# Performance work log

Measured on AMD Instinct MI355X. Metric: run time of the kernel, lower is better.

Reference implementation:

```python
import jax, jax.numpy as jnp
import numpy as np

H = 1024          # hidden_size
NH = 16           # num_attention_heads
HD = H // NH      # head_dim = 64
CAUSAL_HEADS = 4  # causal_attention_heads
META_HEADS = NH // 4
B, S = 2, 2048
CVEC = 16
# static cognitive-state scalars (Python floats in the original dict)
CAUSAL_WEIGHT = 0.7   # > 0.5 -> causal branch active
AWARENESS = 0.9       # > 0.8 -> metacognitive branch active


def _mha(x, in_w, in_b, out_w, out_b, n_heads):
    """torch nn.MultiheadAttention (batch_first, self-attn, no mask, eval).
    in_w: [H, 3H] (pre-transposed), out_w: [H, H]."""
    b, s, h = x.shape
    hd = h // n_heads
    qkv = x @ in_w + in_b                      # [b, s, 3H]
    q, k, v = jnp.split(qkv, 3, axis=-1)
    def heads(t):
        return t.reshape(b, s, n_heads, hd).transpose(0, 2, 1, 3)  # [b, nh, s, hd]
    q, k, v = heads(q), heads(k), heads(v)
    scores = jnp.einsum('bhqd,bhkd->bhqk', q, k) / jnp.sqrt(jnp.float32(hd))
    probs = jax.nn.softmax(scores, axis=-1)
    ctx = jnp.einsum('bhqk,bhkd->bhqd', probs, v)
    ctx = ctx.transpose(0, 2, 1, 3).reshape(b, s, h)
    return ctx @ out_w + out_b


def setup_inputs() -> dict:
    key = jax.random.key(0)
    ks = jax.random.split(key, 20)
    w = lambda k, shp: (jax.random.normal(k, shp, dtype=jnp.float32) * 0.02)
    inp = {
        'hidden_states': jax.random.normal(ks[0], (B, S, H), dtype=jnp.float32),
        'attention_mask': jnp.ones((B, S), dtype=jnp.int32),
        'consciousness_vector': jax.random.uniform(ks[1], (CVEC,), dtype=jnp.float32),
        'Wq': w(ks[2], (H, H)), 'bq': jnp.zeros((H,), jnp.float32),
        'Wk': w(ks[3], (H, H)), 'bk': jnp.zeros((H,), jnp.float32),
        'Wv': w(ks[4], (H, H)), 'bv': jnp.zeros((H,), jnp.float32),
        'Wg': w(ks[5], (H, NH)), 'bg': jnp.zeros((NH,), jnp.float32),
        'Wa': w(ks[6], (CVEC, NH)), 'ba': jnp.zeros((NH,), jnp.float32),
        'ca_in_w': w(ks[7], (H, 3 * H)), 'ca_in_b': jnp.zeros((3 * H,), jnp.float32),
        'ca_out_w': w(ks[8], (H, H)), 'ca_out_b': jnp.zeros((H,), jnp.float32),
        'ma_in_w': w(ks[9], (H, 3 * H)), 'ma_in_b': jnp.zeros((3 * H,), jnp.float32),
        'ma_out_w': w(ks[10], (H, H)), 'ma_out_b': jnp.zeros((H,), jnp.float32),
        'Wo': w(ks[11], (H, H)), 'bo': jnp.zeros((H,), jnp.float32),
    }
    return inp


def reference(hidden_states, attention_mask, consciousness_vector,
              Wq, bq, Wk, bk, Wv, bv, Wg, bg, Wa, ba,
              ca_in_w, ca_in_b, ca_out_w, ca_out_b,
              ma_in_w, ma_in_b, ma_out_w, ma_out_b, Wo, bo):
    b, s, h = hidden_states.shape
    def heads(t):
        return t.reshape(b, s, NH, HD).transpose(0, 2, 1, 3)  # [b, NH, s, HD]
    q = heads(hidden_states @ Wq + bq)
    k = heads(hidden_states @ Wk + bk)
    v = heads(hidden_states @ Wv + bv)
    scores = jnp.einsum('bhqd,bhkd->bhqk', q, k) / jnp.sqrt(jnp.float32(HD))
    # consciousness modulation: sigmoid(gate(hs) + awareness(cvec)) -> [b, s, NH]
    gate = hidden_states @ Wg + bg
    awareness = consciousness_vector @ Wa + ba            # [NH]
    modulation = jax.nn.sigmoid(gate + awareness)         # [b, s, NH]
    # per-head, per-query-row scaling of scores ([b, NH, s, 1])
    scores = scores * modulation.transpose(0, 2, 1)[:, :, :, None]
    # mask: [b, s] -> [b, 1, 1, s]; masked positions -> -inf before softmax
    scores = jnp.where(attention_mask[:, None, None, :] == 0, -jnp.inf, scores)
    probs = jax.nn.softmax(scores, axis=-1)
    # dropout is identity in eval mode
    ctx = jnp.einsum('bhqk,bhkd->bhqd', probs, v)
    ctx = ctx.transpose(0, 2, 1, 3).reshape(b, s, h)
    # causal branch (causal_active > 0.5)
    causal_ctx = _mha(hidden_states, ca_in_w, ca_in_b, ca_out_w, ca_out_b, CAUSAL_HEADS)
    ctx = ctx * (1.0 - CAUSAL_WEIGHT) + causal_ctx * CAUSAL_WEIGHT
    # metacognitive branch (awareness_level > 0.8)
    meta_ctx = _mha(ctx, ma_in_w, ma_in_b, ma_out_w, ma_out_b, META_HEADS)
    mw = (AWARENESS - 0.8) / 0.2
    ctx = ctx * (1.0 - mw * 0.3) + meta_ctx * (mw * 0.3)
    return ctx @ Wo + bo
```

## Files before the change

### kernel.cpp

```cpp
#include <hip/hip_runtime.h>
#include <math.h>

#define HDIM 1024
#define NHEAD 16
#define SEQ   2048
#define BATCH 2
#define NROWS (BATCH * SEQ)
#define NEG_INF (-__builtin_inff())

typedef unsigned short u16;
typedef float  f32x4  __attribute__((ext_vector_type(4)));
typedef short  short8 __attribute__((ext_vector_type(8)));
typedef _Float16 half8 __attribute__((ext_vector_type(8)));
typedef __fp16 fp16x2 __attribute__((ext_vector_type(2)));

__device__ __forceinline__ u16 f2bf(float x) {
    unsigned u = __float_as_uint(x);
    unsigned r = u + 0x7fffu + ((u >> 16) & 1u);
    return (u16)(r >> 16);
}
__device__ __forceinline__ float bf2f(u16 h) { return __uint_as_float(((unsigned)h) << 16); }
__device__ __forceinline__ u16 f2h(float x) { _Float16 h = (_Float16)x; return *(u16*)&h; }
__device__ __forceinline__ unsigned pkh(float a, float b) {
    fp16x2 h = __builtin_amdgcn_cvt_pkrtz(a, b);
    return __builtin_bit_cast(unsigned int, h);
}
__device__ __forceinline__ float ex2(float x) { return __builtin_amdgcn_exp2f(x); }

__global__ __launch_bounds__(256) void conv_f16(const float* __restrict__ src,
                                                u16* __restrict__ dst)
{
    int i8 = (blockIdx.x * 256 + threadIdx.x) * 8;
    float4 a = *(const float4*)&src[i8];
    float4 b = *(const float4*)&src[i8 + 4];
    u16 h[8] = {f2h(a.x), f2h(a.y), f2h(a.z), f2h(a.w),
                f2h(b.x), f2h(b.y), f2h(b.z), f2h(b.w)};
    uint4 p;
    p.x = h[0] | (h[1] << 16); p.y = h[2] | (h[3] << 16);
    p.z = h[4] | (h[5] << 16); p.w = h[6] | (h[7] << 16);
    *(uint4*)&dst[i8] = p;
}

__global__ __launch_bounds__(256) void mask_bias(const int* __restrict__ m,
                                                 float* __restrict__ mb)
{
    int i = blockIdx.x * 256 + threadIdx.x;
    mb[i] = m[i] ? -6.f : NEG_INF;
}

__global__ __launch_bounds__(256) void convW(const float* __restrict__ Wsrc, int ldw, int n0,
                                             int dst, u16* __restrict__ WTH, u16* __restrict__ WTL)
{
    __shared__ float tile[64][65];
    int t = threadIdx.x;
    int nb = blockIdx.x * 64, kb = blockIdx.y * 64;
    #pragma unroll
    for (int i = 0; i < 4; i++) {
        int r = (t >> 4) + i * 16, cg = t & 15;
        float4 v = *(const float4*)&Wsrc[(size_t)(kb + r) * ldw + n0 + nb + cg * 4];
        tile[r][cg * 4 + 0] = v.x; tile[r][cg * 4 + 1] = v.y;
        tile[r][cg * 4 + 2] = v.z; tile[r][cg * 4 + 3] = v.w;
    }
    __syncthreads();
    int n = t & 63, g0 = (t >> 6) * 2;
    #pragma unroll
    for (int gg = 0; gg < 2; gg++) {
        int g = g0 + gg;
        u16 hi[8], lo[8];
        #pragma unroll
        for (int u = 0; u < 8; u++) {
            float x = tile[g * 8 + u][n];
            hi[u] = f2bf(x); lo[u] = f2bf(x - bf2f(hi[u]));
        }
        size_t ob = (size_t)(dst + nb + n) * 1024 + kb + g * 8;
        uint4 ph, pl;
        ph.x = hi[0] | (hi[1] << 16); ph.y = hi[2] | (hi[3] << 16);
        ph.z = hi[4] | (hi[5] << 16); ph.w = hi[6] | (hi[7] << 16);
        pl.x = lo[0] | (lo[1] << 16); pl.y = lo[2] | (lo[3] << 16);
        pl.z = lo[4] | (lo[5] << 16); pl.w = lo[6] | (lo[7] << 16);
        *(uint4*)&WTH[ob] = ph;
        *(uint4*)&WTL[ob] = pl;
    }
}

__global__ __launch_bounds__(256) void convW3_f16(
    const float* __restrict__ w0, const float* __restrict__ w1, const float* __restrict__ w2,
    int ldw, int n0s, u16* __restrict__ WT)
{
    __shared__ float tile[64][65];
    int t = threadIdx.x;
    int z = blockIdx.z;
    const float* Wsrc = (z == 0) ? w0 : (z == 1) ? w1 : w2;
    int n0 = z * n0s, dst = z * 1024;
    int nb = blockIdx.x * 64, kb = blockIdx.y * 64;
    #pragma unroll
    for (int i = 0; i < 4; i++) {
        int r = (t >> 4) + i * 16, cg = t & 15;
        float4 v = *(const float4*)&Wsrc[(size_t)(kb + r) * ldw + n0 + nb + cg * 4];
        tile[r][cg * 4 + 0] = v.x; tile[r][cg * 4 + 1] = v.y;
        tile[r][cg * 4 + 2] = v.z; tile[r][cg * 4 + 3] = v.w;
    }
    __syncthreads();
    int n = t & 63, g0 = (t >> 6) * 2;
    #pragma unroll
    for (int gg = 0; gg < 2; gg++) {
        int g = g0 + gg;
        u16 h[8];
        #pragma unroll
        for (int u = 0; u < 8; u++) h[u] = f2h(tile[g * 8 + u][n]);
        size_t ob = (size_t)(dst + nb + n) * 1024 + kb + g * 8;
        uint4 p;
        p.x = h[0] | (h[1] << 16); p.y = h[2] | (h[3] << 16);
        p.z = h[4] | (h[5] << 16); p.w = h[6] | (h[7] << 16);
        *(uint4*)&WT[ob] = p;
    }
}

__global__ __launch_bounds__(256) void transpose_f16(
    const u16* __restrict__ in, u16* __restrict__ out)
{
    __shared__ u16 th[64][72];
    int t = threadIdx.x;
    int cb = blockIdx.x * 64;
    int rb = blockIdx.y * 64;
    {
        int r = t >> 2;
        #pragma unroll
        for (int i = 0; i < 2; i++) {
            int ck = (t & 3) + 4 * i;
            *(short8*)&th[r][ck * 8] = *(const short8*)&in[(size_t)(rb + r) * 3072 + 2048 + cb + ck * 8];
        }
    }
    __syncthreads();
    int c = t & 63, g0 = (t >> 6) * 2;
    #pragma unroll
    for (int gg = 0; gg < 2; gg++) {
        int g = g0 + gg;
        u16 hv[8];
        #pragma unroll
        for (int u = 0; u < 8; u++) hv[u] = th[g * 8 + u][c];
        size_t ob = (size_t)(cb + c) * NROWS + rb + g * 8;
        uint4 ph;
        ph.x = hv[0] | (hv[1] << 16); ph.y = hv[2] | (hv[3] << 16);
        ph.z = hv[4] | (hv[5] << 16); ph.w = hv[6] | (hv[7] << 16);
        *(uint4*)&out[ob] = ph;
    }
}

__global__ __launch_bounds__(256) void gate_f32(
    const float* __restrict__ hs, const float* __restrict__ Wg,
    const float* __restrict__ bg, const float* __restrict__ cvec,
    const float* __restrict__ Wa, const float* __restrict__ ba,
    float* __restrict__ mod)
{
    __shared__ float aw[16];
    int t = threadIdx.x;
    if (t < 16) {
        float s = ba[t];
        for (int i = 0; i < 16; i++) s = fmaf(cvec[i], Wa[i * 16 + t], s);
        aw[t] = s;
    }
    __syncthreads();
    int h = t & 15;
    int r = blockIdx.x * 16 + (t >> 4);
    const float* hrow = hs + (size_t)r * HDIM;
    float s = bg[h];
    for (int k = 0; k < HDIM; k++) s = fmaf(hrow[k], Wg[k * 16 + h], s);
    s += aw[h];
    mod[(size_t)r * 16 + h] = 1.f / (1.f + __expf(-s));
}

__global__ __launch_bounds__(256, 3) void gemm_f16(
    const u16* __restrict__ A, const u16* __restrict__ BT,
    const float* __restrict__ b0, const float* __restrict__ b1, const float* __restrict__ b2,
    u16* __restrict__ out, int M, int N, int K)
{
    __shared__ u16 aS[128][40], bS[128][40];
    int t = threadIdx.x;
    int l = t & 63, w = t >> 6;
    int lane15 = l & 15, quad = l >> 4;
    int wm = (w >> 1) * 64, wn = (w & 1) * 64;
    int m0 = blockIdx.y * 128, n0 = blockIdx.x * 128;
    int sr = t >> 1;
    f32x4 acc[4][4] = {};
    short8 pa[2], pb[2];
    auto pre = [&](int k0) {
        #pragma unroll
        for (int i = 0; i < 2; i++) {
            int ck = (t & 1) * 2 + i;
            pa[i] = *(const short8*)&A[(size_t)(m0 + sr) * K + k0 + ck * 8];
            pb[i] = *(const short8*)&BT[(size_t)(n0 + sr) * K + k0 + ck * 8];
        }
    };
    pre(0);
    for (int k0 = 0; k0 < K; k0 += 32) {
        __syncthreads();
        #pragma unroll
        for (int i = 0; i < 2; i++) {
            int ck = (t & 1) * 2 + i;
            *(short8*)&aS[sr][ck * 8] = pa[i];
            *(short8*)&bS[sr][ck * 8] = pb[i];
        }
        __syncthreads();
        if (k0 + 32 < K) pre(k0 + 32);
        half8 af[4], bf[4];
        #pragma unroll
        for (int mt = 0; mt < 4; mt++)
            af[mt] = *(const half8*)&aS[wm + mt * 16 + lane15][quad * 8];
        #pragma unroll
        for (int nt = 0; nt < 4; nt++)
            bf[nt] = *(const half8*)&bS[wn + nt * 16 + lane15][quad * 8];
        #pragma unroll
        for (int mt = 0; mt < 4; mt++)
            #pragma unroll
            for (int nt = 0; nt < 4; nt++)
                acc[mt][nt] = __builtin_amdgcn_mfma_f32_16x16x32_f16(af[mt], bf[nt], acc[mt][nt], 0, 0, 0);
    }
    #pragma unroll
    for (int nt = 0; nt < 4; nt++) {
        int col = n0 + wn + nt * 16 + lane15;
        const float* bsel = (col < 1024) ? b0 : (col < 2048) ? b1 : b2;
        float bv = bsel[col & 1023];
        #pragma unroll
        for (int mt = 0; mt < 4; mt++)
            #pragma unroll
            for (int reg = 0; reg < 4; reg++) {
                int row = m0 + wm + mt * 16 + quad * 4 + reg;
                out[(size_t)row * N + col] = f2h(acc[mt][nt][reg] + bv);
            }
    }
}

__global__ __launch_bounds__(256, 2) void gemm_bf3(
    const u16* __restrict__ AH, const u16* __restrict__ AL,
    const u16* __restrict__ BTH, const u16* __restrict__ BTL,
    const float* __restrict__ bias,
    const u16* __restrict__ CinH, const u16* __restrict__ CinL,
    float* __restrict__ outF, u16* __restrict__ outH, u16* __restrict__ outL,
    u16* __restrict__ outX,
    int M, int N, int K, float alpha, float beta, int omode)
{
    __shared__ u16 aH[128][40], aL[128][40], bH[128][40], bL[128][40];
    int t = threadIdx.x;
    int l = t & 63, w = t >> 6;
    int lane15 = l & 15, quad = l >> 4;
    int wm = (w >> 1) * 64, wn = (w & 1) * 64;
    int m0 = blockIdx.y * 128, n0 = blockIdx.x * 128;
    int sr = t >> 1;
    f32x4 acc[4][4] = {};
    short8 pah[2], pal[2], pbh[2], pbl[2];

    auto pre = [&](int k0) {
        #pragma unroll
        for (int i = 0; i < 2; i++) {
            int ck = (t & 1) * 2 + i;
            size_t ga = (size_t)(m0 + sr) * K + k0 + ck * 8;
            size_t gb = (size_t)(n0 + sr) * K + k0 + ck * 8;
            pah[i] = *(const short8*)&AH[ga];
            pal[i] = *(const short8*)&AL[ga];
            pbh[i] = *(const short8*)&BTH[gb];
            pbl[i] = *(const short8*)&BTL[gb];
        }
    };
    pre(0);
    for (int k0 = 0; k0 < K; k0 += 32) {
        __syncthreads();
        #pragma unroll
        for (int i = 0; i < 2; i++) {
            int ck = (t & 1) * 2 + i;
            *(short8*)&aH[sr][ck * 8] = pah[i];
            *(short8*)&aL[sr][ck * 8] = pal[i];
            *(short8*)&bH[sr][ck * 8] = pbh[i];
            *(short8*)&bL[sr][ck * 8] = pbl[i];
        }
        __syncthreads();
        if (k0 + 32 < K) pre(k0 + 32);
        short8 afh[4], afl[4], bfh[4], bfl[4];
        #pragma unroll
        for (int mt = 0; mt < 4; mt++) {
            int r = wm + mt * 16 + lane15;
            afh[mt] = *(const short8*)&aH[r][quad * 8];
            afl[mt] = *(const short8*)&aL[r][quad * 8];
        }
        #pragma unroll
        for (int nt = 0; nt < 4; nt++) {
            int r = wn + nt * 16 + lane15;
            bfh[nt] = *(const short8*)&bH[r][quad * 8];
            bfl[nt] = *(const short8*)&bL[r][quad * 8];
        }
        #pragma unroll
        for (int mt = 0; mt < 4; mt++)
            #pragma unroll
            for (int nt = 0; nt < 4; nt++) {
                acc[mt][nt] = __builtin_amdgcn_mfma_f32_16x16x32_bf16(afh[mt], bfh[nt], acc[mt][nt], 0, 0, 0);
                acc[mt][nt] = __builtin_amdgcn_mfma_f32_16x16x32_bf16(afh[mt], bfl[nt], acc[mt][nt], 0, 0, 0);
                acc[mt][nt] = __builtin_amdgcn_mfma_f32_16x16x32_bf16(afl[mt], bfh[nt], acc[mt][nt], 0, 0, 0);
            }
    }
    #pragma unroll
    for (int nt = 0; nt < 4; nt++) {
        int col = n0 + wn + nt * 16 + lane15;
        float bv = bias[col];
        #pragma unroll
        for (int mt = 0; mt < 4; mt++) {
            #pragma unroll
            for (int reg = 0; reg < 4; reg++) {
                int row = m0 + wm + mt * 16 + quad * 4 + reg;
                size_t idx = (size_t)row * N + col;
                float v = alpha * (acc[mt][nt][reg] + bv);
                if (beta != 0.f) v += beta * (bf2f(CinH[idx]) + bf2f(CinL[idx]));
                if (omode == 0) outF[idx] = v;
                else {
                    u16 hb = f2bf(v);
                    outH[idx] = hb;
                    outL[idx] = f2bf(v - bf2f(hb));
                }
                if (outX) outX[idx] = f2h(v);
            }
        }
    }
}

__global__ __launch_bounds__(256, 4) void attn_main(
    const u16* __restrict__ QKV, const u16* __restrict__ VT,
    const float* __restrict__ modp, const float* __restrict__ mbias, float scale,
    u16* __restrict__ outH, u16* __restrict__ outL)
{
    constexpr int NT = SEQ / 64;
    constexpr int LD = 3 * HDIM;
    __shared__ __align__(16) u16 kb[2][64][64];
    __shared__ __align__(16) u16 vb[2][64][64];
    __shared__ __align__(16) u16 st[4][16][64];

    int t = threadIdx.x, l = t & 63, w = t >> 6;
    int lane15 = l & 15, quad = l >> 4;
    int qt0 = blockIdx.x * 64, h = blockIdx.y, b = blockIdx.z;
    int bS_ = b * SEQ;
    int sr = t >> 2, ck0 = (t & 3) * 2;
    int swz = (lane15 & 7) << 3;

    half8 qf[2];
    {
        size_t qoff = (size_t)(bS_ + qt0 + w * 16 + lane15) * LD + h * 64 + quad * 8;
        qf[0] = *(const half8*)&QKV[qoff];
        qf[1] = *(const half8*)&QKV[qoff + 32];
    }
    float smod2 = scale * 1.44269504f *
                  modp[(size_t)(bS_ + qt0 + w * 16 + lane15) * NHEAD + h];
    float lst = 0.f;
    f32x4 o[4] = {};

    short8 phK[2], phV[2];
    auto loadKV = [&](int kt) {
        size_t baseK = (size_t)(bS_ + kt + sr) * LD + HDIM + h * 64;
        phK[0] = *(const short8*)&QKV[baseK + ck0 * 8];
        phK[1] = *(const short8*)&QKV[baseK + (ck0 + 1) * 8];
        size_t baseV = (size_t)(h * 64 + sr) * NROWS + bS_ + kt;
        phV[0] = *(const short8*)&VT[baseV + ck0 * 8];
        phV[1] = *(const short8*)&VT[baseV + (ck0 + 1) * 8];
    };
    auto stage = [&](int pb_) {
        #pragma unroll
        for (int i = 0; i < 2; i++) {
            int cw = (ck0 + i) ^ (sr & 7);
            *(short8*)&kb[pb_][sr][cw * 8] = phK[i];
            *(short8*)&vb[pb_][sr][cw * 8] = phV[i];
        }
    };

    loadKV(0);

    for (int it = 0; it < NT; it++) {
        int kt = it * 64, pb = it & 1;
        stage(pb);
        __syncthreads();
        if (it + 1 < NT) loadKV(kt + 64);
        f32x4 sacc[4] = {};
        #pragma unroll
        for (int ks = 0; ks < 2; ks++)
            #pragma unroll
            for (int nb = 0; nb < 4; nb++) {
                int r = nb * 16 + lane15;
                int cw = (ks * 4 + quad) ^ (r & 7);
                half8 kf = *(const half8*)&kb[pb][r][cw * 8];
                sacc[nb] = __builtin_amdgcn_mfma_f32_16x16x32_f16(kf, qf[ks], sacc[nb], 0, 0, 0);
            }
        #pragma unroll
        for (int nb = 0; nb < 4; nb++) {
            float4 mb = *(const float4*)&mbias[bS_ + kt + nb * 16 + quad * 4];
            float p0 = ex2(fmaf(sacc[nb][0], smod2, mb.x));
            float p1 = ex2(fmaf(sacc[nb][1], smod2, mb.y));
            float p2 = ex2(fmaf(sacc[nb][2], smod2, mb.z));
            float p3 = ex2(fmaf(sacc[nb][3], smod2, mb.w));
            lst += (p0 + p1) + (p2 + p3);
            uint2 u2;
            u2.x = pkh(p0, p1);
            u2.y = pkh(p2, p3);
            *(uint2*)&st[w][lane15][(nb * 16 + quad * 4) ^ swz] = u2;
        }
        half8 pf[2];
        #pragma unroll
        for (int ks = 0; ks < 2; ks++)
            pf[ks] = *(const half8*)&st[w][lane15][(ks * 32 + quad * 8) ^ swz];
        #pragma unroll
        for (int ks = 0; ks < 2; ks++)
            #pragma unroll
            for (int nb = 0; nb < 4; nb++) {
                int r = nb * 16 + lane15;
                int cw = (ks * 4 + quad) ^ (r & 7);
                half8 vv = *(const half8*)&vb[pb][r][cw * 8];
                o[nb] = __builtin_amdgcn_mfma_f32_16x16x32_f16(pf[ks], vv, o[nb], 0, 0, 0);
            }
    }
    lst += __shfl_xor(lst, 16, 64);
    lst += __shfl_xor(lst, 32, 64);
    #pragma unroll
    for (int reg = 0; reg < 4; reg++) {
        float lv = __shfl(lst, quad * 4 + reg, 64);
        float inv = (lv > 0.f) ? 1.f / lv : 0.f;
        int row = qt0 + w * 16 + quad * 4 + reg;
        size_t rbase = (size_t)(bS_ + row) * HDIM + h * 64;
        #pragma unroll
        for (int nb = 0; nb < 4; nb++) {
            float v = o[nb][reg] * inv;
            size_t idx = rbase + nb * 16 + lane15;
            u16 hb = f2bf(v);
            outH[idx] = hb;
            outL[idx] = f2bf(v - bf2f(hb));
        }
    }
}

template <int NC>
__global__ __launch_bounds__(256, 2) void attn_f16(
    const u16* __restrict__ QKV, const u16* __restrict__ VT,
    float scale, u16* __restrict__ outH, u16* __restrict__ outL, int ldo)
{
    constexpr int HDT = NC * 64;
    constexpr int NT  = (SEQ / 2) / 64;
    constexpr int LD  = 3 * HDIM;
    __shared__ __align__(16) u16 kbuf[2][2][64][64];
    __shared__ __align__(16) u16 st[4][16][68];
    __shared__ float xl[2][16];

    int t = threadIdx.x, l = t & 63, w = t >> 6;
    int lane15 = l & 15, quad = l >> 4;
    int g = w & 1, s = w >> 1;
    int t128 = t & 127, srow = t128 >> 1, ckb = (t128 & 1) * 4;
    int qt0 = blockIdx.x * 32, h = blockIdx.y, b = blockIdx.z;
    int bS = b * SEQ, kbeg = s * (SEQ / 2);

    half8 qf[NC][2];
    {
        size_t qoff = (size_t)(bS + qt0 + g * 16 + lane15) * LD + h * HDT + quad * 8;
        #pragma unroll
        for (int c = 0; c < NC; c++)
            #pragma unroll
            for (int ks = 0; ks < 2; ks++)
                qf[c][ks] = *(const half8*)&QKV[qoff + c * 64 + ks * 32];
    }
    float sc2 = scale * 1.44269504f;
    float lst = 0.f;
    f32x4 o[NC][4] = {};

    short8 phv[4];
    auto loadK = [&](int c, int kt) {
        size_t base = (size_t)(bS + kt + srow) * LD + HDIM + h * HDT + c * 64;
        #pragma unroll
        for (int i = 0; i < 4; i++) phv[i] = *(const short8*)&QKV[base + (ckb + i) * 8];
    };
    auto loadV = [&](int c, int kt) {
        size_t base = (size_t)(h * HDT + c * 64 + srow) * NROWS + bS + kt;
        #pragma unroll
        for (int i = 0; i < 4; i++) phv[i] = *(const short8*)&VT[base + (ckb + i) * 8];
    };
    auto stor = [&](int pb_) {
        #pragma unroll
        for (int i = 0; i < 4; i++) {
            int ck = ckb + i, cw = ck ^ (srow & 7);
            *(short8*)&kbuf[pb_][s][srow][cw * 8] = phv[i];
        }
    };

    loadK(0, kbeg);
    stor(0);
    loadK(1, kbeg);
    int pb = 0;

    for (int it = 0; it < NT; it++) {
        int kt = kbeg + it * 64;
        f32x4 sacc[4] = {};
        #pragma unroll
        for (int c = 0; c < NC; c++) {
            __syncthreads();
            stor(pb ^ 1);
            if (c + 2 < NC) loadK(c + 2, kt);
            else if (c + 2 < 2 * NC) loadV(c + 2 - NC, kt);
            else if (it + 1 < NT) loadK(0, kt + 64);
            #pragma unroll
            for (int ks = 0; ks < 2; ks++)
                #pragma unroll
                for (int nb = 0; nb < 4; nb++) {
                    int r = nb * 16 + lane15;
                    int cw = (ks * 4 + quad) ^ (r & 7);
                    half8 kf = *(const half8*)&kbuf[pb][s][r][cw * 8];
                    sacc[nb] = __builtin_amdgcn_mfma_f32_16x16x32_f16(kf, qf[c][ks], sacc[nb], 0, 0, 0);
                }
            pb ^= 1;
        }
        #pragma unroll
        for (int nb = 0; nb < 4; nb++) {
            float p0 = ex2(fmaf(sacc[nb][0], sc2, -6.f));
            float p1 = ex2(fmaf(sacc[nb][1], sc2, -6.f));
            float p2 = ex2(fmaf(sacc[nb][2], sc2, -6.f));
            float p3 = ex2(fmaf(sacc[nb][3], sc2, -6.f));
            lst += (p0 + p1) + (p2 + p3);
            uint2 u2;
            u2.x = pkh(p0, p1);
            u2.y = pkh(p2, p3);
            *(uint2*)&st[w][lane15][nb * 16 + quad * 4] = u2;
        }
        half8 pf[2];
        #pragma unroll
        for (int ks = 0; ks < 2; ks++)
            pf[ks] = *(const half8*)&st[w][lane15][ks * 32 + quad * 8];
        #pragma unroll
        for (int c = 0; c < NC; c++) {
            __syncthreads();
            if (it < NT - 1 || c < NC - 1) stor(pb ^ 1);
            if (c + 2 < NC) loadV(c + 2, kt);
            else if (it + 1 < NT) {
                int p2 = c + 2 - NC;
                if (p2 < NC) loadK(p2, kt + 64); else loadV(p2 - NC, kt + 64);
            }
            #pragma unroll
            for (int ks = 0; ks < 2; ks++)
                #pragma unroll
                for (int nb = 0; nb < 4; nb++) {
                    int r = nb * 16 + lane15;
                    int cw = (ks * 4 + quad) ^ (r & 7);
                    half8 vv = *(const half8*)&kbuf[pb][s][r][cw * 8];
                    o[c][nb] = __builtin_amdgcn_mfma_f32_16x16x32_f16(pf[ks], vv, o[c][nb], 0, 0, 0);
                }
            pb ^= 1;
        }
    }
    lst += __shfl_xor(lst, 16, 64);
    lst += __shfl_xor(lst, 32, 64);
    float* xO = (float*)kbuf;
    __syncthreads();
    if (s == 1) {
        #pragma unroll
        for (int c = 0; c < NC; c++)
            #pragma unroll
            for (int nb = 0; nb < 4; nb++)
                #pragma unroll
                for (int reg = 0; reg < 4; reg++)
                    xO[(size_t)(g * 16 + quad * 4 + reg) * HDT + c * 64 + nb * 16 + lane15] = o[c][nb][reg];
        if (quad == 0) xl[g][lane15] = lst;
    }
    __syncthreads();
    if (s == 0) {
        #pragma unroll
        for (int reg = 0; reg < 4; reg++) {
            float lt = __shfl(lst, quad * 4 + reg, 64) + xl[g][quad * 4 + reg];
            float inv = (lt > 0.f) ? 1.f / lt : 0.f;
            int row = qt0 + g * 16 + quad * 4 + reg;
            size_t rbase = (size_t)(bS + row) * ldo + h * HDT;
            #pragma unroll
            for (int c = 0; c < NC; c++)
                #pragma unroll
                for (int nb = 0; nb < 4; nb++) {
                    float x1 = xO[(size_t)(g * 16 + quad * 4 + reg) * HDT + c * 64 + nb * 16 + lane15];
                    float v = (o[c][nb][reg] + x1) * inv;
                    size_t idx = rbase + c * 64 + nb * 16 + lane15;
                    u16 hb = f2bf(v);
                    outH[idx] = hb;
                    outL[idx] = f2bf(v - bf2f(hb));
                }
        }
    }
}

extern "C" void kernel_launch(void* const* d_in, const int* in_sizes, int n_in,
                              void* d_out, int out_size, void* d_ws, size_t ws_size,
                              hipStream_t stream)
{
    const float* hs   = (const float*)d_in[0];
    const int*   mask = (const int*)d_in[1];
    const float* cvec = (const float*)d_in[2];
    const float* Wq = (const float*)d_in[3];  const float* bq = (const float*)d_in[4];
    const float* Wk = (const float*)d_in[5];  const float* bk = (const float*)d_in[6];
    const float* Wv = (const float*)d_in[7];  const float* bv = (const float*)d_in[8];
    const float* Wg = (const float*)d_in[9];  const float* bg = (const float*)d_in[10];
    const float* Wa = (const float*)d_in[11]; const float* ba = (const float*)d_in[12];
    const float* caw = (const float*)d_in[13]; const float* cab = (const float*)d_in[14];
    const float* cow = (const float*)d_in[15]; const float* cob = (const float*)d_in[16];
    const float* maw = (const float*)d_in[17]; const float* mab = (const float*)d_in[18];
    const float* mow = (const float*)d_in[19]; const float* mob = (const float*)d_in[20];
    const float* Wo = (const float*)d_in[21]; const float* bo = (const float*)d_in[22];
    float* out = (float*)d_out;

    char* W = (char*)d_ws;
    const size_t MB = (size_t)1 << 20;
    u16*  QKV  = (u16*)(W + 0 * MB);
    u16*  VT   = (u16*)(W + 24 * MB);
    u16*  ctxH = (u16*)(W + 32 * MB);    u16* ctxL = (u16*)(W + 40 * MB);
    u16*  C2H  = (u16*)(W + 48 * MB);    u16* C2L  = (u16*)(W + 56 * MB);
    float* MOD = (float*)(W + 64 * MB);
    u16*  hsX  = (u16*)(W + 65 * MB);
    u16*  ctxX = (u16*)(W + 73 * MB);
    u16*  wtX  = (u16*)(W + 81 * MB);
    u16*  wtH  = (u16*)(W + 87 * MB);    u16* wtL = (u16*)(W + 89 * MB);
    float* MB_ = (float*)(W + 91 * MB);

    dim3 blk(256);
    dim3 gw(16, 16);
    dim3 gw3(16, 16, 3);
    dim3 gt(16, 64);
    dim3 gg3(24, 32);
    dim3 gg1(8, 32);
    dim3 gaM(SEQ / 64, NHEAD, BATCH);
    dim3 gaB(SEQ / 32, 4, BATCH);

    conv_f16<<<2048, blk, 0, stream>>>(hs, hsX);
    mask_bias<<<NROWS / 256, blk, 0, stream>>>(mask, MB_);
    gate_f32<<<NROWS / 16, blk, 0, stream>>>(hs, Wg, bg, cvec, Wa, ba, MOD);

    convW3_f16<<<gw3, blk, 0, stream>>>(Wq, Wk, Wv, 1024, 0, wtX);
    gemm_f16<<<gg3, blk, 0, stream>>>(hsX, wtX, bq, bk, bv, QKV, NROWS, 3072, 1024);
    transpose_f16<<<gt, blk, 0, stream>>>(QKV, VT);
    attn_main<<<gaM, blk, 0, stream>>>(QKV, VT, MOD, MB_, 0.125f, ctxH, ctxL);

    convW3_f16<<<gw3, blk, 0, stream>>>(caw, caw, caw, 3072, 1024, wtX);
    gemm_f16<<<gg3, blk, 0, stream>>>(hsX, wtX, cab, cab + 1024, cab + 2048, QKV, NROWS, 3072, 1024);
    transpose_f16<<<gt, blk, 0, stream>>>(QKV, VT);
    attn_f16<4><<<gaB, blk, 0, stream>>>(QKV, VT, 0.0625f, C2H, C2L, HDIM);
    convW<<<gw, blk, 0, stream>>>(cow, 1024, 0, 0, wtH, wtL);
    gemm_bf3<<<gg1, blk, 0, stream>>>(C2H, C2L, wtH, wtL, cob,
        ctxH, ctxL, nullptr, ctxH, ctxL, ctxX, NROWS, 1024, 1024, 0.7f, 0.3f, 1);

    convW3_f16<<<gw3, blk, 0, stream>>>(maw, maw, maw, 3072, 1024, wtX);
    gemm_f16<<<gg3, blk, 0, stream>>>(ctxX, wtX, mab, mab + 1024, mab + 2048, QKV, NROWS, 3072, 1024);
    transpose_f16<<<gt, blk, 0, stream>>>(QKV, VT);
    attn_f16<4><<<gaB, blk, 0, stream>>>(QKV, VT, 0.0625f, C2H, C2L, HDIM);
    convW<<<gw, blk, 0, stream>>>(mow, 1024, 0, 0, wtH, wtL);
    gemm_bf3<<<gg1, blk, 0, stream>>>(C2H, C2L, wtH, wtL, mob,
        ctxH, ctxL, nullptr, ctxH, ctxL, nullptr, NROWS, 1024, 1024, 0.15f, 0.85f, 1);

    convW<<<gw, blk, 0, stream>>>(Wo, 1024, 0, 0, wtH, wtL);
    gemm_bf3<<<gg1, blk, 0, stream>>>(ctxH, ctxL, wtH, wtL, bo,
        nullptr, nullptr, out, nullptr, nullptr, nullptr, NROWS, 1024, 1024, 1.f, 0.f, 0);
}
```

Baseline: 691.3 us.

## Load K and V fragments directly from global memory in attn_f16, dropping LDS staging

The attention kernel stops staging K and V tiles through a double-buffered LDS buffer with per-chunk __syncthreads, and has each wave load its MFMA operands straight from global memory instead. The K loop hardcodes four 64-wide chunks, so it assumes NC==4. The P staging buffer loses its padding and gets an XOR swizzle to avoid bank conflicts, and xO becomes its own shared array. This removes the block barriers and LDS traffic but gives up cross-wave reuse, which means more global or L2 traffic and exposed load latency. It would be wrong for NC other than 4.

```diff
diff --git a/kernel.cpp b/kernel.cpp
--- a/kernel.cpp
+++ b/kernel.cpp
@@ -439,16 +439,16 @@
     constexpr int HDT = NC * 64;
     constexpr int NT  = (SEQ / 2) / 64;
     constexpr int LD  = 3 * HDIM;
-    __shared__ __align__(16) u16 kbuf[2][2][64][64];
-    __shared__ __align__(16) u16 st[4][16][68];
+    __shared__ __align__(16) u16 st[4][16][64];
+    __shared__ float xO[32][HDT];
     __shared__ float xl[2][16];
 
     int t = threadIdx.x, l = t & 63, w = t >> 6;
     int lane15 = l & 15, quad = l >> 4;
     int g = w & 1, s = w >> 1;
-    int t128 = t & 127, srow = t128 >> 1, ckb = (t128 & 1) * 4;
     int qt0 = blockIdx.x * 32, h = blockIdx.y, b = blockIdx.z;
     int bS = b * SEQ, kbeg = s * (SEQ / 2);
+    int swz = (lane15 & 7) << 3;
 
     half8 qf[NC][2];
     {
@@ -463,50 +463,28 @@
     float lst = 0.f;
     f32x4 o[NC][4] = {};
 
-    short8 phv[4];
-    auto loadK = [&](int c, int kt) {
-        size_t base = (size_t)(bS + kt + srow) * LD + HDIM + h * HDT + c * 64;
-        #pragma unroll
-        for (int i = 0; i < 4; i++) phv[i] = *(const short8*)&QKV[base + (ckb + i) * 8];
-    };
-    auto loadV = [&](int c, int kt) {
-        size_t base = (size_t)(h * HDT + c * 64 + srow) * NROWS + bS + kt;
-        #pragma unroll
-        for (int i = 0; i < 4; i++) phv[i] = *(const short8*)&VT[base + (ckb + i) * 8];
-    };
-    auto stor = [&](int pb_) {
-        #pragma unroll
-        for (int i = 0; i < 4; i++) {
-            int ck = ckb + i, cw = ck ^ (srow & 7);
-            *(short8*)&kbuf[pb_][s][srow][cw * 8] = phv[i];
-        }
-    };
-
-    loadK(0, kbeg);
-    stor(0);
-    loadK(1, kbeg);
-    int pb = 0;
-
     for (int it = 0; it < NT; it++) {
         int kt = kbeg + it * 64;
         f32x4 sacc[4] = {};
         #pragma unroll
-        for (int c = 0; c < NC; c++) {
-            __syncthreads();
-            stor(pb ^ 1);
-            if (c + 2 < NC) loadK(c + 2, kt);
-            else if (c + 2 < 2 * NC) loadV(c + 2 - NC, kt);
-            else if (it + 1 < NT) loadK(0, kt + 64);
-            #pragma unroll
-            for (int ks = 0; ks < 2; ks++)
-                #pragma unroll
-                for (int nb = 0; nb < 4; nb++) {
-                    int r = nb * 16 + lane15;
-                    int cw = (ks * 4 + quad) ^ (r & 7);
-                    half8 kf = *(const half8*)&kbuf[pb][s][r][cw * 8];
-                    sacc[nb] = __builtin_amdgcn_mfma_f32_16x16x32_f16(kf, qf[c][ks], sacc[nb], 0, 0, 0);
-                }
-            pb ^= 1;
+        for (int nb = 0; nb < 4; nb++) {
+            const u16* kr = &QKV[(size_t)(bS + kt + nb * 16 + lane15) * LD + HDIM + h * HDT + quad * 8];
+            half8 k0 = *(const half8*)&kr[0];
+            half8 k1 = *(const half8*)&kr[32];
+            half8 k2 = *(const half8*)&kr[64];
+            half8 k3 = *(const half8*)&kr[96];
+            half8 k4 = *(const half8*)&kr[128];
+            half8 k5 = *(const half8*)&kr[160];
+            half8 k6 = *(const half8*)&kr[192];
+            half8 k7 = *(const half8*)&kr[224];
+            sacc[nb] = __builtin_amdgcn_mfma_f32_16x16x32_f16(k0, qf[0][0], sacc[nb], 0, 0, 0);
+            sacc[nb] = __builtin_amdgcn_mfma_f32_16x16x32_f16(k1, qf[0][1], sacc[nb], 0, 0, 0);
+            sacc[nb] = __builtin_amdgcn_mfma_f32_16x16x32_f16(k2, qf[1][0], sacc[nb], 0, 0, 0);
+            sacc[nb] = __builtin_amdgcn_mfma_f32_16x16x32_f16(k3, qf[1][1], sacc[nb], 0, 0, 0);
+            sacc[nb] = __builtin_amdgcn_mfma_f32_16x16x32_f16(k4, qf[2][0], sacc[nb], 0, 0, 0);
+            sacc[nb] = __builtin_amdgcn_mfma_f32_16x16x32_f16(k5, qf[2][1], sacc[nb], 0, 0, 0);
+            sacc[nb] = __builtin_amdgcn_mfma_f32_16x16x32_f16(k6, qf[3][0], sacc[nb], 0, 0, 0);
+            sacc[nb] = __builtin_amdgcn_mfma_f32_16x16x32_f16(k7, qf[3][1], sacc[nb], 0, 0, 0);
         }
         #pragma unroll
         for (int nb = 0; nb < 4; nb++) {
@@ -518,36 +496,25 @@
             uint2 u2;
             u2.x = pkh(p0, p1);
             u2.y = pkh(p2, p3);
-            *(uint2*)&st[w][lane15][nb * 16 + quad * 4] = u2;
+            *(uint2*)&st[w][lane15][(nb * 16 + quad * 4) ^ swz] = u2;
         }
         half8 pf[2];
         #pragma unroll
         for (int ks = 0; ks < 2; ks++)
-            pf[ks] = *(const half8*)&st[w][lane15][ks * 32 + quad * 8];
-        #pragma unroll
-        for (int c = 0; c < NC; c++) {
-            __syncthreads();
-            if (it < NT - 1 || c < NC - 1) stor(pb ^ 1);
-            if (c + 2 < NC) loadV(c + 2, kt);
-            else if (it + 1 < NT) {
-                int p2 = c + 2 - NC;
-                if (p2 < NC) loadK(p2, kt + 64); else loadV(p2 - NC, kt + 64);
+            pf[ks] = *(const half8*)&st[w][lane15][(ks * 32 + quad * 8) ^ swz];
+        #pragma unroll
+        for (int c = 0; c < NC; c++)
+            #pragma unroll
+            for (int nb = 0; nb < 4; nb++) {
+                const u16* vr = &VT[(size_t)(h * HDT + c * 64 + nb * 16 + lane15) * NROWS + bS + kt + quad * 8];
+                half8 v0 = *(const half8*)&vr[0];
+                half8 v1 = *(const half8*)&vr[32];
+                o[c][nb] = __builtin_amdgcn_mfma_f32_16x16x32_f16(pf[0], v0, o[c][nb], 0, 0, 0);
+                o[c][nb] = __builtin_amdgcn_mfma_f32_16x16x32_f16(pf[1], v1, o[c][nb], 0, 0, 0);
             }
-            #pragma unroll
-            for (int ks = 0; ks < 2; ks++)
-                #pragma unroll
-                for (int nb = 0; nb < 4; nb++) {
-                    int r = nb * 16 + lane15;
-                    int cw = (ks * 4 + quad) ^ (r & 7);
-                    half8 vv = *(const half8*)&kbuf[pb][s][r][cw * 8];
-                    o[c][nb] = __builtin_amdgcn_mfma_f32_16x16x32_f16(pf[ks], vv, o[c][nb], 0, 0, 0);
-                }
-            pb ^= 1;
-        }
     }
     lst += __shfl_xor(lst, 16, 64);
     lst += __shfl_xor(lst, 32, 64);
-    float* xO = (float*)kbuf;
     __syncthreads();
     if (s == 1) {
         #pragma unroll
@@ -556,7 +523,7 @@
             for (int nb = 0; nb < 4; nb++)
                 #pragma unroll
                 for (int reg = 0; reg < 4; reg++)
-                    xO[(size_t)(g * 16 + quad * 4 + reg) * HDT + c * 64 + nb * 16 + lane15] = o[c][nb][reg];
+                    xO[g * 16 + quad * 4 + reg][c * 64 + nb * 16 + lane15] = o[c][nb][reg];
         if (quad == 0) xl[g][lane15] = lst;
     }
     __syncthreads();
@@ -571,7 +538,7 @@
             for (int c = 0; c < NC; c++)
                 #pragma unroll
                 for (int nb = 0; nb < 4; nb++) {
-                    float x1 = xO[(size_t)(g * 16 + quad * 4 + reg) * HDT + c * 64 + nb * 16 + lane15];
+                    float x1 = xO[g * 16 + quad * 4 + reg][c * 64 + nb * 16 + lane15];
                     float v = (o[c][nb][reg] + x1) * inv;
                     size_t idx = rbase + c * 64 + nb * 16 + lane15;
                     u16 hb = f2bf(v);
```

Result: slower. 1.078 ms (+55.9%).

## Stage two head-dim chunks per barrier in attention K/V pipeline

Applied to the files above, without the earlier changes.

The attention kernel now loads and stores two 64-wide head-dim chunks of K or V per pipeline stage, doubling the shared-memory buffer, so each iteration needs four barriers instead of 2*NC. The code is hardcoded for NC=4. The P staging tile drops its padding and uses an XOR swizzle to avoid bank conflicts. In exchange it uses more LDS and more registers (8 short8 prefetch registers), which can lower occupancy under launch_bounds(256,2).

```diff
diff --git a/kernel.cpp b/kernel.cpp
--- a/kernel.cpp
+++ b/kernel.cpp
@@ -439,8 +439,8 @@
     constexpr int HDT = NC * 64;
     constexpr int NT  = (SEQ / 2) / 64;
     constexpr int LD  = 3 * HDIM;
-    __shared__ __align__(16) u16 kbuf[2][2][64][64];
-    __shared__ __align__(16) u16 st[4][16][68];
+    __shared__ __align__(16) u16 kbuf[2][2][2][64][64];
+    __shared__ __align__(16) u16 st[4][16][64];
     __shared__ float xl[2][16];
 
     int t = threadIdx.x, l = t & 63, w = t >> 6;
@@ -449,6 +449,7 @@
     int t128 = t & 127, srow = t128 >> 1, ckb = (t128 & 1) * 4;
     int qt0 = blockIdx.x * 32, h = blockIdx.y, b = blockIdx.z;
     int bS = b * SEQ, kbeg = s * (SEQ / 2);
+    int swz = (lane15 & 7) << 3;
 
     half8 qf[NC][2];
     {
@@ -463,51 +464,73 @@
     float lst = 0.f;
     f32x4 o[NC][4] = {};
 
-    short8 phv[4];
-    auto loadK = [&](int c, int kt) {
+    short8 phv[8];
+    auto loadK2 = [&](int c, int kt) {
         size_t base = (size_t)(bS + kt + srow) * LD + HDIM + h * HDT + c * 64;
         #pragma unroll
         for (int i = 0; i < 4; i++) phv[i] = *(const short8*)&QKV[base + (ckb + i) * 8];
+        #pragma unroll
+        for (int i = 0; i < 4; i++) phv[4 + i] = *(const short8*)&QKV[base + 64 + (ckb + i) * 8];
     };
-    auto loadV = [&](int c, int kt) {
+    auto loadV2 = [&](int c, int kt) {
         size_t base = (size_t)(h * HDT + c * 64 + srow) * NROWS + bS + kt;
         #pragma unroll
         for (int i = 0; i < 4; i++) phv[i] = *(const short8*)&VT[base + (ckb + i) * 8];
+        size_t base2 = base + (size_t)64 * NROWS;
+        #pragma unroll
+        for (int i = 0; i < 4; i++) phv[4 + i] = *(const short8*)&VT[base2 + (ckb + i) * 8];
     };
-    auto stor = [&](int pb_) {
+    auto stor2 = [&](int pb_) {
         #pragma unroll
         for (int i = 0; i < 4; i++) {
-            int ck = ckb + i, cw = ck ^ (srow & 7);
-            *(short8*)&kbuf[pb_][s][srow][cw * 8] = phv[i];
+            int cw = (ckb + i) ^ (srow & 7);
+            *(short8*)&kbuf[pb_][s][0][srow][cw * 8] = phv[i];
+        }
+        #pragma unroll
+        for (int i = 0; i < 4; i++) {
+            int cw = (ckb + i) ^ (srow & 7);
+            *(short8*)&kbuf[pb_][s][1][srow][cw * 8] = phv[4 + i];
         }
     };
 
-    loadK(0, kbeg);
-    stor(0);
-    loadK(1, kbeg);
+    loadK2(0, kbeg);
+    stor2(0);
+    loadK2(2, kbeg);
     int pb = 0;
 
     for (int it = 0; it < NT; it++) {
         int kt = kbeg + it * 64;
         f32x4 sacc[4] = {};
-        #pragma unroll
-        for (int c = 0; c < NC; c++) {
-            __syncthreads();
-            stor(pb ^ 1);
-            if (c + 2 < NC) loadK(c + 2, kt);
-            else if (c + 2 < 2 * NC) loadV(c + 2 - NC, kt);
-            else if (it + 1 < NT) loadK(0, kt + 64);
+        __syncthreads();
+        stor2(pb ^ 1);
+        loadV2(0, kt);
+        #pragma unroll
+        for (int j = 0; j < 2; j++)
             #pragma unroll
             for (int ks = 0; ks < 2; ks++)
                 #pragma unroll
                 for (int nb = 0; nb < 4; nb++) {
                     int r = nb * 16 + lane15;
                     int cw = (ks * 4 + quad) ^ (r & 7);
-                    half8 kf = *(const half8*)&kbuf[pb][s][r][cw * 8];
-                    sacc[nb] = __builtin_amdgcn_mfma_f32_16x16x32_f16(kf, qf[c][ks], sacc[nb], 0, 0, 0);
+                    half8 kf = *(const half8*)&kbuf[pb][s][j][r][cw * 8];
+                    sacc[nb] = __builtin_amdgcn_mfma_f32_16x16x32_f16(kf, qf[j][ks], sacc[nb], 0, 0, 0);
                 }
-            pb ^= 1;
-        }
+        pb ^= 1;
+        __syncthreads();
+        stor2(pb ^ 1);
+        loadV2(2, kt);
+        #pragma unroll
+        for (int j = 0; j < 2; j++)
+            #pragma unroll
+            for (int ks = 0; ks < 2; ks++)
+                #pragma unroll
+                for (int nb = 0; nb < 4; nb++) {
+                    int r = nb * 16 + lane15;
+                    int cw = (ks * 4 + quad) ^ (r & 7);
+                    half8 kf = *(const half8*)&kbuf[pb][s][j][r][cw * 8];
+                    sacc[nb] = __builtin_amdgcn_mfma_f32_16x16x32_f16(kf, qf[2 + j][ks], sacc[nb], 0, 0, 0);
+                }
+        pb ^= 1;
         #pragma unroll
         for (int nb = 0; nb < 4; nb++) {
             float p0 = ex2(fmaf(sacc[nb][0], sc2, -6.f));
@@ -518,32 +541,41 @@
             uint2 u2;
             u2.x = pkh(p0, p1);
             u2.y = pkh(p2, p3);
-            *(uint2*)&st[w][lane15][nb * 16 + quad * 4] = u2;
+            *(uint2*)&st[w][lane15][(nb * 16 + quad * 4) ^ swz] = u2;
         }
         half8 pf[2];
         #pragma unroll
         for (int ks = 0; ks < 2; ks++)
-            pf[ks] = *(const half8*)&st[w][lane15][ks * 32 + quad * 8];
-        #pragma unroll
-        for (int c = 0; c < NC; c++) {
-            __syncthreads();
-            if (it < NT - 1 || c < NC - 1) stor(pb ^ 1);
-            if (c + 2 < NC) loadV(c + 2, kt);
-            else if (it + 1 < NT) {
-                int p2 = c + 2 - NC;
-                if (p2 < NC) loadK(p2, kt + 64); else loadV(p2 - NC, kt + 64);
-            }
+            pf[ks] = *(const half8*)&st[w][lane15][(ks * 32 + quad * 8) ^ swz];
+        __syncthreads();
+        stor2(pb ^ 1);
+        if (it + 1 < NT) loadK2(0, kt + 64);
+        #pragma unroll
+        for (int j = 0; j < 2; j++)
             #pragma unroll
             for (int ks = 0; ks < 2; ks++)
                 #pragma unroll
                 for (int nb = 0; nb < 4; nb++) {
                     int r = nb * 16 + lane15;
                     int cw = (ks * 4 + quad) ^ (r & 7);
-                    half8 vv = *(const half8*)&kbuf[pb][s][r][cw * 8];
-                    o[c][nb] = __builtin_amdgcn_mfma_f32_16x16x32_f16(pf[ks], vv, o[c][nb], 0, 0, 0);
+                    half8 vv = *(const half8*)&kbuf[pb][s][j][r][cw * 8];
+                    o[j][nb] = __builtin_amdgcn_mfma_f32_16x16x32_f16(pf[ks], vv, o[j][nb], 0, 0, 0);
                 }
-            pb ^= 1;
-        }
+        pb ^= 1;
+        __syncthreads();
+        if (it + 1 < NT) { stor2(pb ^ 1); loadK2(2, kt + 64); }
+        #pragma unroll
+        for (int j = 0; j < 2; j++)
+            #pragma unroll
+            for (int ks = 0; ks < 2; ks++)
+                #pragma unroll
+                for (int nb = 0; nb < 4; nb++) {
+                    int r = nb * 16 + lane15;
+                    int cw = (ks * 4 + quad) ^ (r & 7);
+                    half8 vv = *(const half8*)&kbuf[pb][s][j][r][cw * 8];
+                    o[2 + j][nb] = __builtin_amdgcn_mfma_f32_16x16x32_f16(pf[ks], vv, o[2 + j][nb], 0, 0, 0);
+                }
+        pb ^= 1;
     }
     lst += __shfl_xor(lst, 16, 64);
     lst += __shfl_xor(lst, 32, 64);
```

Measured after the change: 695.8 us. No clear change (+0.7%).

## Load GEMM tiles straight to LDS via global_load_lds, drop register prefetch

Applied to the files above, without the earlier changes.

Both GEMM kernels now copy A/B tiles from global memory directly into LDS with the global_load_lds builtin, in place of staging them through registers with a one-step prefetch. The LDS rows lose their padding (stride 32 instead of 40), and gemm_bf3's launch bound is raised to 3 blocks per SM. This frees the VGPRs used for staging, which may allow higher occupancy. In exchange, the load/compute overlap from register double-buffering is gone, each iteration waits on a direct load followed by a barrier, and the unpadded layout may cause LDS bank conflicts on fragment reads.

```diff
diff --git a/kernel.cpp b/kernel.cpp
--- a/kernel.cpp
+++ b/kernel.cpp
@@ -26,6 +26,9 @@
     return __builtin_bit_cast(unsigned int, h);
 }
 __device__ __forceinline__ float ex2(float x) { return __builtin_amdgcn_exp2f(x); }
+__device__ __forceinline__ void gl_lds16(const u16* g, u16* l) {
+    __builtin_amdgcn_global_load_lds((const void*)g, (void*)l, 16, 0, 0);
+}
 
 __global__ __launch_bounds__(256) void conv_f16(const float* __restrict__ src,
                                                 u16* __restrict__ dst)
@@ -175,34 +178,26 @@
     const float* __restrict__ b0, const float* __restrict__ b1, const float* __restrict__ b2,
     u16* __restrict__ out, int M, int N, int K)
 {
-    __shared__ u16 aS[128][40], bS[128][40];
+    __shared__ u16 aS[128][32], bS[128][32];
     int t = threadIdx.x;
     int l = t & 63, w = t >> 6;
     int lane15 = l & 15, quad = l >> 4;
     int wm = (w >> 1) * 64, wn = (w & 1) * 64;
     int m0 = blockIdx.y * 128, n0 = blockIdx.x * 128;
-    int sr = t >> 1;
+    int grow = w * 32 + (l >> 2);
+    int gcol = (l & 3) * 8;
     f32x4 acc[4][4] = {};
-    short8 pa[2], pb[2];
-    auto pre = [&](int k0) {
-        #pragma unroll
-        for (int i = 0; i < 2; i++) {
-            int ck = (t & 1) * 2 + i;
-            pa[i] = *(const short8*)&A[(size_t)(m0 + sr) * K + k0 + ck * 8];
-            pb[i] = *(const short8*)&BT[(size_t)(n0 + sr) * K + k0 + ck * 8];
-        }
-    };
-    pre(0);
+
     for (int k0 = 0; k0 < K; k0 += 32) {
         __syncthreads();
         #pragma unroll
-        for (int i = 0; i < 2; i++) {
-            int ck = (t & 1) * 2 + i;
-            *(short8*)&aS[sr][ck * 8] = pa[i];
-            *(short8*)&bS[sr][ck * 8] = pb[i];
+        for (int j = 0; j < 2; j++) {
+            gl_lds16(&A[(size_t)(m0 + grow + j * 16) * K + k0 + gcol],
+                     &aS[w * 32 + j * 16][0]);
+            gl_lds16(&BT[(size_t)(n0 + grow + j * 16) * K + k0 + gcol],
+                     &bS[w * 32 + j * 16][0]);
         }
         __syncthreads();
-        if (k0 + 32 < K) pre(k0 + 32);
         half8 af[4], bf[4];
         #pragma unroll
         for (int mt = 0; mt < 4; mt++)
@@ -231,7 +226,7 @@
     }
 }
 
-__global__ __launch_bounds__(256, 2) void gemm_bf3(
+__global__ __launch_bounds__(256, 3) void gemm_bf3(
     const u16* __restrict__ AH, const u16* __restrict__ AL,
     const u16* __restrict__ BTH, const u16* __restrict__ BTL,
     const float* __restrict__ bias,
@@ -240,41 +235,29 @@
     u16* __restrict__ outX,
     int M, int N, int K, float alpha, float beta, int omode)
 {
-    __shared__ u16 aH[128][40], aL[128][40], bH[128][40], bL[128][40];
+    __shared__ u16 aH[128][32], aL[128][32], bH[128][32], bL[128][32];
     int t = threadIdx.x;
     int l = t & 63, w = t >> 6;
     int lane15 = l & 15, quad = l >> 4;
     int wm = (w >> 1) * 64, wn = (w & 1) * 64;
     int m0 = blockIdx.y * 128, n0 = blockIdx.x * 128;
-    int sr = t >> 1;
+    int grow = w * 32 + (l >> 2);
+    int gcol = (l & 3) * 8;
     f32x4 acc[4][4] = {};
-    short8 pah[2], pal[2], pbh[2], pbl[2];
-
-    auto pre = [&](int k0) {
-        #pragma unroll
-        for (int i = 0; i < 2; i++) {
-            int ck = (t & 1) * 2 + i;
-            size_t ga = (size_t)(m0 + sr) * K + k0 + ck * 8;
-            size_t gb = (size_t)(n0 + sr) * K + k0 + ck * 8;
-            pah[i] = *(const short8*)&AH[ga];
-            pal[i] = *(const short8*)&AL[ga];
-            pbh[i] = *(const short8*)&BTH[gb];
-            pbl[i] = *(const short8*)&BTL[gb];
-        }
-    };
-    pre(0);
+
     for (int k0 = 0; k0 < K; k0 += 32) {
         __syncthreads();
         #pragma unroll
-        for (int i = 0; i < 2; i++) {
-            int ck = (t & 1) * 2 + i;
-            *(short8*)&aH[sr][ck * 8] = pah[i];
-            *(short8*)&aL[sr][ck * 8] = pal[i];
-            *(short8*)&bH[sr][ck * 8] = pbh[i];
-            *(short8*)&bL[sr][ck * 8] = pbl[i];
+        for (int j = 0; j < 2; j++) {
+            size_t ga = (size_t)(m0 + grow + j * 16) * K + k0 + gcol;
+            size_t gb = (size_t)(n0 + grow + j * 16) * K + k0 + gcol;
+            int lr = w * 32 + j * 16;
+            gl_lds16(&AH[ga],  &aH[lr][0]);
+            gl_lds16(&AL[ga],  &aL[lr][0]);
+            gl_lds16(&BTH[gb], &bH[lr][0]);
+            gl_lds16(&BTL[gb], &bL[lr][0]);
         }
         __syncthreads();
-        if (k0 + 32 < K) pre(k0 + 32);
         short8 afh[4], afl[4], bfh[4], bfl[4];
         #pragma unroll
         for (int mt = 0; mt < 4; mt++) {
```

Result: no change. 696.2 us (+0.7%).
